# Optimization experiments

Hardware: AMD Instinct MI355X
Metric: run time of the kernel (lower is better)

Reference implementation:

```python
import jax, jax.numpy as jnp
import numpy as np

BETA = 0.5

def setup_inputs() -> dict:
    key = jax.random.key(0)
    ks = jax.random.split(key, 12)
    B, H, d, hid = 2048, 100, 128, 256
    item_num, region_num, dist_num = 100000, 1000, 16
    return {
        "history": jax.random.randint(ks[0], (B, H), 0, item_num),
        "target": jax.random.randint(ks[1], (B,), 0, item_num),
        "history_region": jax.random.randint(ks[2], (B, H), 0, region_num),
        "target_region": jax.random.randint(ks[3], (B,), 0, region_num),
        "target_distance": jax.random.uniform(ks[4], (B,), dtype=jnp.float32),
        "E_hist": jax.random.normal(ks[5], (item_num, d), dtype=jnp.float32) * 0.01,
        "E_tgt": jax.random.normal(ks[6], (item_num, d), dtype=jnp.float32) * 0.01,
        "E_reg": jax.random.normal(ks[7], (region_num, d), dtype=jnp.float32) * 0.01,
        "E_dist": jax.random.normal(ks[8], (dist_num, d), dtype=jnp.float32) * 0.01,
        "W1": jax.random.normal(ks[9], (hid, 2 * d), dtype=jnp.float32) * 0.05,
        "b1": jnp.zeros((hid,), dtype=jnp.float32),
        "w2": jax.random.normal(ks[10], (hid,), dtype=jnp.float32) * 0.05,
    }

def reference(history, target, history_region, target_region, target_distance,
              E_hist, E_tgt, E_reg, E_dist, W1, b1, w2):
    # history embeddings: [B,H,2d]
    hist = jnp.concatenate([E_hist[history], E_reg[history_region]], axis=-1)
    # target embeddings: [B,1,2d]
    tgt = jnp.concatenate([E_tgt[target], E_reg[target_region]], axis=-1)[:, None, :]
    x = hist * tgt                                   # [B,H,2d]
    a = jax.nn.relu(jnp.einsum('bhd,kd->bhk', x, W1) + b1)  # [B,H,hid]
    score = jnp.einsum('bhk,k->bh', a, w2)           # [B,H]
    # distance bias: scalar per batch element
    dist = jnp.sum(target_distance[:, None] * E_dist[0], axis=1)  # [B]
    exp_A = jnp.exp(score + dist[:, None])           # [B,H]
    mask = (history != target[:, None]).astype(exp_A.dtype)
    exp_A = exp_A * mask
    exp_sum = jnp.power(jnp.sum(exp_A, axis=-1), BETA)  # [B]
    attn = exp_A / exp_sum[:, None]                  # [B,H]
    # weighted inner product: sum_h sum_d attn*hist*tgt
    pred = jnp.sum(hist * attn[:, :, None] * tgt, axis=(1, 2))  # [B]
    return jax.nn.sigmoid(pred)
```

## Files before the change

### kernel.cpp

```cpp
#include <hip/hip_runtime.h>
#include <stdint.h>

typedef __attribute__((ext_vector_type(8))) short bf16x8;
typedef __attribute__((ext_vector_type(4))) float f32x4;

#define HH  100
#define DD  128
#define HID 256
#define NT  7

__device__ __forceinline__ unsigned short f2bf(float f) {
    unsigned int u = __float_as_uint(f);
    u += 0x7fffu + ((u >> 16) & 1u);
    return (unsigned short)(u >> 16);
}

__global__ void w1_pack(const float* __restrict__ W1, unsigned short* __restrict__ W1p) {
    int unit = blockIdx.x * 256 + threadIdx.x;
    int lane = unit & 63;
    int s    = (unit >> 6) & 7;
    int st   = unit >> 9;
    int col  = lane & 15, quad = lane >> 4;
    const float* src = W1 + (size_t)(st * 16 + col) * HID + s * 32 + quad * 8;
    union { unsigned short u[8]; bf16x8 v; } o;
    #pragma unroll
    for (int j = 0; j < 8; j++) o.u[j] = f2bf(src[j]);
    *(bf16x8*)(W1p + (size_t)unit * 8) = o.v;
}

__device__ __forceinline__ unsigned int cvt_pk_bf16(float lo, float hi) {
    unsigned int r;
    asm("v_cvt_pk_bf16_f32 %0, %1, %2" : "=v"(r) : "v"(lo), "v"(hi));
    return r;
}

#define CONSUME(V0, V1, S, AP, TGT, ACC) do {                                     \
    const float* tp_ = (TGT) + (S) * 32 + quad * 8;                               \
    float4 t0_ = *(const float4*)tp_, t1_ = *(const float4*)(tp_ + 4);            \
    float x0=(V0).x*t0_.x, x1=(V0).y*t0_.y, x2=(V0).z*t0_.z, x3=(V0).w*t0_.w;     \
    float x4=(V1).x*t1_.x, x5=(V1).y*t1_.y, x6=(V1).z*t1_.z, x7=(V1).w*t1_.w;     \
    (ACC) += (x0+x1)+(x2+x3)+((x4+x5)+(x6+x7));                                   \
    union { unsigned int u[4]; int4 v; } fb_;                                     \
    fb_.u[0]=cvt_pk_bf16(x0,x1); fb_.u[1]=cvt_pk_bf16(x2,x3);                     \
    fb_.u[2]=cvt_pk_bf16(x4,x5); fb_.u[3]=cvt_pk_bf16(x6,x7);                     \
    *(int4*)((AP) + (size_t)((S) * 64 + lane) * 8) = fb_.v;                       \
} while (0)

#define MFMA_PAIR(MM0, MM1) do {                                                  \
    int m0_ = (MM0); if (m0_ >= NT) m0_ -= NT;                                    \
    int m1_ = (MM1); if (m1_ >= NT) m1_ -= NT;                                    \
    const unsigned short* a0p_ = Ab + m0_ * 4096;                                 \
    const unsigned short* a1p_ = Ab + m1_ * 4096;                                 \
    f32x4 c00_={0,0,0,0}, c01_={0,0,0,0}, c10_={0,0,0,0}, c11_={0,0,0,0};         \
    _Pragma("unroll")                                                             \
    for (int s_ = 0; s_ < 8; s_++) {                                              \
        bf16x8 x0_ = *(const bf16x8*)(a0p_ + (size_t)(s_ * 64 + lane) * 8);       \
        bf16x8 x1_ = *(const bf16x8*)(a1p_ + (size_t)(s_ * 64 + lane) * 8);       \
        c00_ = __builtin_amdgcn_mfma_f32_16x16x32_bf16(w1f[s_],     x0_, c00_, 0,0,0); \
        c01_ = __builtin_amdgcn_mfma_f32_16x16x32_bf16(w1f[8 + s_], x0_, c01_, 0,0,0); \
        c10_ = __builtin_amdgcn_mfma_f32_16x16x32_bf16(w1f[s_],     x1_, c10_, 0,0,0); \
        c11_ = __builtin_amdgcn_mfma_f32_16x16x32_bf16(w1f[8 + s_], x1_, c11_, 0,0,0); \
    }                                                                             \
    float sp0_ = 0.f, sp1_ = 0.f;                                                 \
    _Pragma("unroll")                                                             \
    for (int r_ = 0; r_ < 4; r_++) {                                              \
        float z00_=c00_[r_]+bb0[r_], z01_=c01_[r_]+bb1[r_];                       \
        float z10_=c10_[r_]+bb0[r_], z11_=c11_[r_]+bb1[r_];                       \
        sp0_ += ((z00_>0.f)?z00_*ww0[r_]:0.f) + ((z01_>0.f)?z01_*ww1[r_]:0.f);    \
        sp1_ += ((z10_>0.f)?z10_*ww0[r_]:0.f) + ((z11_>0.f)?z11_*ww1[r_]:0.f);    \
    }                                                                             \
    sp0_ += __shfl_xor(sp0_, 16); sp0_ += __shfl_xor(sp0_, 32);                   \
    sp1_ += __shfl_xor(sp1_, 16); sp1_ += __shfl_xor(sp1_, 32);                   \
    if (quad == 0) {                                                              \
        scorep[wave][m0_ * 16 + col] = sp0_;                                      \
        scorep[wave][m1_ * 16 + col] = sp1_;                                      \
    }                                                                             \
} while (0)

#define MFMA_SINGLE(MM0) do {                                                     \
    int m0_ = (MM0); if (m0_ >= NT) m0_ -= NT;                                    \
    const unsigned short* a0p_ = Ab + m0_ * 4096;                                 \
    f32x4 c00_={0,0,0,0}, c01_={0,0,0,0};                                         \
    _Pragma("unroll")                                                             \
    for (int s_ = 0; s_ < 8; s_++) {                                              \
        bf16x8 x0_ = *(const bf16x8*)(a0p_ + (size_t)(s_ * 64 + lane) * 8);       \
        c00_ = __builtin_amdgcn_mfma_f32_16x16x32_bf16(w1f[s_],     x0_, c00_, 0,0,0); \
        c01_ = __builtin_amdgcn_mfma_f32_16x16x32_bf16(w1f[8 + s_], x0_, c01_, 0,0,0); \
    }                                                                             \
    float sp0_ = 0.f;                                                             \
    _Pragma("unroll")                                                             \
    for (int r_ = 0; r_ < 4; r_++) {                                              \
        float z00_=c00_[r_]+bb0[r_], z01_=c01_[r_]+bb1[r_];                       \
        sp0_ += ((z00_>0.f)?z00_*ww0[r_]:0.f) + ((z01_>0.f)?z01_*ww1[r_]:0.f);    \
    }                                                                             \
    sp0_ += __shfl_xor(sp0_, 16); sp0_ += __shfl_xor(sp0_, 32);                   \
    if (quad == 0) scorep[wave][m0_ * 16 + col] = sp0_;                           \
} while (0)

__global__ __launch_bounds__(512, 2) void nais_kernel(
    const int* __restrict__ history,
    const int* __restrict__ target,
    const int* __restrict__ history_region,
    const int* __restrict__ target_region,
    const float* __restrict__ target_distance,
    const float* __restrict__ E_hist,
    const float* __restrict__ E_tgt,
    const float* __restrict__ E_reg,
    const float* __restrict__ E_dist,
    const float* __restrict__ b1,
    const float* __restrict__ w2,
    const unsigned short* __restrict__ W1p,
    float* __restrict__ out,
    int Btot)
{
    __shared__ __align__(16) unsigned short As[2][NT * 4096];
    __shared__ __align__(16) float tgts3[3][HID];
    __shared__ __align__(16) float b1s[HID];
    __shared__ __align__(16) float w2s[HID];
    __shared__ __align__(16) int   hidx3[3][HH];
    __shared__ __align__(16) int   hreg3[3][HH];
    __shared__ __align__(16) float scorep[8][112];
    __shared__ __align__(16) float xsum2[2][112];
    __shared__ int   tgA[64];
    __shared__ int   trA[64];
    __shared__ float tdA[64];
    __shared__ float p12[2][4];
    __shared__ float s_sumE;

    const int t    = threadIdx.x;
    const int lane = t & 63;
    const int wave = t >> 6;
    const int col  = lane & 15;
    const int quad = lane >> 4;

    const int NB   = (Btot + gridDim.x - 1) / gridDim.x;
    const int base = blockIdx.x * NB;
    int cnt = Btot - base;
    if (cnt <= 0) return;
    if (cnt > NB) cnt = NB;

    if (t < cnt) {
        tgA[t] = target[base + t];
        trA[t] = target_region[base + t];
        tdA[t] = target_distance[base + t];
    }
    if (wave == 4) {
        *(float4*)(b1s + lane * 4) = *(const float4*)(b1 + lane * 4);
        *(float4*)(w2s + lane * 4) = *(const float4*)(w2 + lane * 4);
    }
    if (wave == 5) {
        float v = E_dist[lane] + E_dist[64 + lane];
        #pragma unroll
        for (int off = 32; off; off >>= 1) v += __shfl_xor(v, off);
        if (lane == 0) s_sumE = v;
    }
    __syncthreads();

    bf16x8 w1f[16];
    #pragma unroll
    for (int i = 0; i < 16; i++) {
        const int unit = ((2 * wave + (i >> 3)) * 8 + (i & 7)) * 64 + lane;
        w1f[i] = *(const bf16x8*)(W1p + (size_t)unit * 8);
    }
    #pragma unroll
    for (int i = 0; i < 16; i++) asm volatile("" : "+v"(w1f[i]));

    if (wave < 2 && wave < cnt) {
        const int em = base + wave;
        int4 mh = {0,0,0,0}, mr = {0,0,0,0};
        if (lane < 25)      mh = *(const int4*)(history + (size_t)em * HH + lane * 4);
        else if (lane < 50) mr = *(const int4*)(history_region + (size_t)em * HH + (lane - 25) * 4);
        const int tg2 = tgA[wave], tr2 = trA[wave];
        const float* tp2 = (lane < 32) ? (E_tgt + (size_t)tg2 * DD + lane * 4)
                                       : (E_reg + (size_t)tr2 * DD + (lane - 32) * 4);
        float4 mt4 = *(const float4*)tp2;
        if (lane < 25)      *(int4*)&hidx3[wave][lane * 4] = mh;
        else if (lane < 50) *(int4*)&hreg3[wave][(lane - 25) * 4] = mr;
        *(float4*)&tgts3[wave][lane * 4] = mt4;
    }
    __syncthreads();

    if (wave < NT) {
        const int row0 = wave * 16 + col;
        const int rc  = (row0 < HH) ? row0 : row0 - 64;
        const int ih  = hidx3[0][rc];
        const int ir  = hreg3[0][rc];
        const float* ph = E_hist + (size_t)ih * DD + quad * 8;
        const float* pr = E_reg  + (size_t)ir * DD + quad * 8;
        unsigned short* ap = &As[0][wave * 4096];
        float4 g[16];
        #pragma unroll
        for (int s = 0; s < 4; s++) {
            g[2*s]     = *(const float4*)(ph + s * 32);
            g[2*s + 1] = *(const float4*)(ph + s * 32 + 4);
            g[8 + 2*s] = *(const float4*)(pr + s * 32);
            g[9 + 2*s] = *(const float4*)(pr + s * 32 + 4);
        }
        float acc = 0.f;
        #pragma unroll
        for (int s = 0; s < 8; s++) CONSUME(g[2*s], g[2*s+1], s, ap, tgts3[0], acc);
        float v = acc;
        v += __shfl_xor(v, 16);
        v += __shfl_xor(v, 32);
        if (quad == 0) xsum2[0][row0] = v;
    }

    const int st0 = 2 * wave;
    const f32x4 bb0 = *(const f32x4*)&b1s[st0 * 16 + quad * 4];
    const f32x4 bb1 = *(const f32x4*)&b1s[st0 * 16 + 16 + quad * 4];
    const f32x4 ww0 = *(const f32x4*)&w2s[st0 * 16 + quad * 4];
    const f32x4 ww1 = *(const f32x4*)&w2s[st0 * 16 + 16 + quad * 4];

    __syncthreads();

    int cur = 0, cm = 0, nm = 1, n2 = 2;

    #pragma unroll 1
    for (int i = 0; i < cnt; i++) {
        const bool do_g = (i + 1 < cnt) && (wave < NT);
        const bool do_m = (i + 2 < cnt) && (wave == 7);

        float4 g[16];
        int row0 = 0;
        if (do_g) {
            row0 = wave * 16 + col;
            const int rc = (row0 < HH) ? row0 : row0 - 64;
            const int ih = hidx3[nm][rc];
            const int ir = hreg3[nm][rc];
            const float* ph = E_hist + (size_t)ih * DD + quad * 8;
            const float* pr = E_reg  + (size_t)ir * DD + quad * 8;
            #pragma unroll
            for (int s = 0; s < 4; s++) {
                g[2*s]     = *(const float4*)(ph + s * 32);
                g[2*s + 1] = *(const float4*)(ph + s * 32 + 4);
                g[8 + 2*s] = *(const float4*)(pr + s * 32);
                g[9 + 2*s] = *(const float4*)(pr + s * 32 + 4);
            }
        }
        int4 mh = {0,0,0,0}, mr4 = {0,0,0,0};
        float4 mt4 = {0.f, 0.f, 0.f, 0.f};
        if (do_m) {
            const int em = base + i + 2;
            if (lane < 25)      mh  = *(const int4*)(history + (size_t)em * HH + lane * 4);
            else if (lane < 50) mr4 = *(const int4*)(history_region + (size_t)em * HH + (lane - 25) * 4);
            const int tg2 = tgA[i + 2], tr2 = trA[i + 2];
            const float* tp2 = (lane < 32) ? (E_tgt + (size_t)tg2 * DD + lane * 4)
                                           : (E_reg + (size_t)tr2 * DD + (lane - 32) * 4);
            mt4 = *(const float4*)tp2;
        }

        const unsigned short* Ab = &As[cur][0];

        MFMA_PAIR(wave,     wave + 1);
        MFMA_PAIR(wave + 2, wave + 3);
        MFMA_PAIR(wave + 4, wave + 5);
        MFMA_SINGLE(wave + 6);

        __syncthreads();

        {
            float sc = 0.f;
            if (t < 112) {
                #pragma unroll
                for (int w = 0; w < 8; w++) sc += scorep[w][t];
            }
            float e1v = 0.f, e2v = 0.f;
            if (t < HH) {
                const float dist = tdA[i] * s_sumE;
                if (hidx3[cm][t] != tgA[i]) {
                    float e = expf(sc + dist);
                    e1v = e;
                    e2v = e * xsum2[cur][t];
                }
            }
            if (wave < 2) {
                #pragma unroll
                for (int off = 32; off; off >>= 1) {
                    e1v += __shfl_xor(e1v, off);
                    e2v += __shfl_xor(e2v, off);
                }
                if (lane == 0) {
                    p12[cur][wave]     = e1v;
                    p12[cur][2 + wave] = e2v;
                }
            }
            if (i > 0 && t == 128) {
                float s1 = p12[cur ^ 1][0] + p12[cur ^ 1][1];
                float s2 = p12[cur ^ 1][2] + p12[cur ^ 1][3];
                float pred = s2 / sqrtf(s1);
                out[base + i - 1] = 1.f / (1.f + expf(-pred));
            }
        }

        if (do_g) {
            unsigned short* An = &As[cur ^ 1][wave * 4096];
            const float* tgt = &tgts3[nm][0];
            float acc = 0.f;
            #pragma unroll
            for (int s = 0; s < 8; s++) CONSUME(g[2*s], g[2*s+1], s, An, tgt, acc);
            float v = acc;
            v += __shfl_xor(v, 16);
            v += __shfl_xor(v, 32);
            if (quad == 0) xsum2[cur ^ 1][row0] = v;
        } else if (do_m) {
            if (lane < 25)      *(int4*)&hidx3[n2][lane * 4] = mh;
            else if (lane < 50) *(int4*)&hreg3[n2][(lane - 25) * 4] = mr4;
            *(float4*)&tgts3[n2][lane * 4] = mt4;
        }

        __syncthreads();
        cur ^= 1;
        const int tmp = cm; cm = nm; nm = n2; n2 = tmp;
    }

    if (t == 0) {
        const int sl = (cnt - 1) & 1;
        float s1 = p12[sl][0] + p12[sl][1];
        float s2 = p12[sl][2] + p12[sl][3];
        float pred = s2 / sqrtf(s1);
        out[base + cnt - 1] = 1.f / (1.f + expf(-pred));
    }
}

extern "C" void kernel_launch(void* const* d_in, const int* in_sizes, int n_in,
                              void* d_out, int out_size, void* d_ws, size_t ws_size,
                              hipStream_t stream) {
    const int*   history         = (const int*)d_in[0];
    const int*   target          = (const int*)d_in[1];
    const int*   history_region  = (const int*)d_in[2];
    const int*   target_region   = (const int*)d_in[3];
    const float* target_distance = (const float*)d_in[4];
    const float* E_hist          = (const float*)d_in[5];
    const float* E_tgt           = (const float*)d_in[6];
    const float* E_reg           = (const float*)d_in[7];
    const float* E_dist          = (const float*)d_in[8];
    const float* W1              = (const float*)d_in[9];
    const float* b1              = (const float*)d_in[10];
    const float* w2              = (const float*)d_in[11];

    unsigned short* W1p = (unsigned short*)d_ws;
    const int B = in_sizes[1];

    int grid = (B + 7) / 8;
    if (grid > 256) grid = 256;

    w1_pack<<<32, 256, 0, stream>>>(W1, W1p);
    nais_kernel<<<grid, 512, 0, stream>>>(history, target, history_region, target_region,
                                          target_distance, E_hist, E_tgt, E_reg, E_dist,
                                          b1, w2, W1p, (float*)d_out, B);
}
```

Baseline: 185.8 us.

## Deepen software pipeline to one barrier per iteration and interleave MFMA with gather consume

```diff
diff --git a/kernel.cpp b/kernel.cpp
--- a/kernel.cpp
+++ b/kernel.cpp
@@ -72,8 +72,8 @@
     sp0_ += __shfl_xor(sp0_, 16); sp0_ += __shfl_xor(sp0_, 32);                   \
     sp1_ += __shfl_xor(sp1_, 16); sp1_ += __shfl_xor(sp1_, 32);                   \
     if (quad == 0) {                                                              \
-        scorep[wave][m0_ * 16 + col] = sp0_;                                      \
-        scorep[wave][m1_ * 16 + col] = sp1_;                                      \
+        scp[m0_ * 16 + col] = sp0_;                                               \
+        scp[m1_ * 16 + col] = sp1_;                                               \
     }                                                                             \
 } while (0)
 
@@ -94,7 +94,7 @@
         sp0_ += ((z00_>0.f)?z00_*ww0[r_]:0.f) + ((z01_>0.f)?z01_*ww1[r_]:0.f);    \
     }                                                                             \
     sp0_ += __shfl_xor(sp0_, 16); sp0_ += __shfl_xor(sp0_, 32);                   \
-    if (quad == 0) scorep[wave][m0_ * 16 + col] = sp0_;                           \
+    if (quad == 0) scp[m0_ * 16 + col] = sp0_;                                    \
 } while (0)
 
 __global__ __launch_bounds__(512, 2) void nais_kernel(
@@ -114,13 +114,13 @@
     int Btot)
 {
     __shared__ __align__(16) unsigned short As[2][NT * 4096];
-    __shared__ __align__(16) float tgts3[3][HID];
+    __shared__ __align__(16) float tgts4[4][HID];
     __shared__ __align__(16) float b1s[HID];
     __shared__ __align__(16) float w2s[HID];
-    __shared__ __align__(16) int   hidx3[3][HH];
-    __shared__ __align__(16) int   hreg3[3][HH];
-    __shared__ __align__(16) float scorep[8][112];
-    __shared__ __align__(16) float xsum2[2][112];
+    __shared__ __align__(16) int   hidx4[4][HH];
+    __shared__ __align__(16) int   hreg4[4][HH];
+    __shared__ __align__(16) float scorep[2][8][112];
+    __shared__ __align__(16) float xsumR[3][112];
     __shared__ int   tgA[64];
     __shared__ int   trA[64];
     __shared__ float tdA[64];
@@ -174,17 +174,17 @@
         const float* tp2 = (lane < 32) ? (E_tgt + (size_t)tg2 * DD + lane * 4)
                                        : (E_reg + (size_t)tr2 * DD + (lane - 32) * 4);
         float4 mt4 = *(const float4*)tp2;
-        if (lane < 25)      *(int4*)&hidx3[wave][lane * 4] = mh;
-        else if (lane < 50) *(int4*)&hreg3[wave][(lane - 25) * 4] = mr;
-        *(float4*)&tgts3[wave][lane * 4] = mt4;
+        if (lane < 25)      *(int4*)&hidx4[wave][lane * 4] = mh;
+        else if (lane < 50) *(int4*)&hreg4[wave][(lane - 25) * 4] = mr;
+        *(float4*)&tgts4[wave][lane * 4] = mt4;
     }
     __syncthreads();
 
     if (wave < NT) {
         const int row0 = wave * 16 + col;
         const int rc  = (row0 < HH) ? row0 : row0 - 64;
-        const int ih  = hidx3[0][rc];
-        const int ir  = hreg3[0][rc];
+        const int ih  = hidx4[0][rc];
+        const int ir  = hreg4[0][rc];
         const float* ph = E_hist + (size_t)ih * DD + quad * 8;
         const float* pr = E_reg  + (size_t)ir * DD + quad * 8;
         unsigned short* ap = &As[0][wave * 4096];
@@ -198,11 +198,11 @@
         }
         float acc = 0.f;
         #pragma unroll
-        for (int s = 0; s < 8; s++) CONSUME(g[2*s], g[2*s+1], s, ap, tgts3[0], acc);
+        for (int s = 0; s < 8; s++) CONSUME(g[2*s], g[2*s+1], s, ap, tgts4[0], acc);
         float v = acc;
         v += __shfl_xor(v, 16);
         v += __shfl_xor(v, 32);
-        if (quad == 0) xsum2[0][row0] = v;
+        if (quad == 0) xsumR[0][row0] = v;
     }
 
     const int st0 = 2 * wave;
@@ -213,20 +213,22 @@
 
     __syncthreads();
 
-    int cur = 0, cm = 0, nm = 1, n2 = 2;
-
     #pragma unroll 1
-    for (int i = 0; i < cnt; i++) {
+    for (int i = 0; i < cnt + 2; i++) {
+        const int  ii   = i & 1;
+        const bool do_f = (i < cnt);
         const bool do_g = (i + 1 < cnt) && (wave < NT);
         const bool do_m = (i + 2 < cnt) && (wave == 7);
+        const bool do_s = (i >= 1) && (i <= cnt);
 
         float4 g[16];
         int row0 = 0;
         if (do_g) {
+            const int ms = (i + 1) & 3;
             row0 = wave * 16 + col;
             const int rc = (row0 < HH) ? row0 : row0 - 64;
-            const int ih = hidx3[nm][rc];
-            const int ir = hreg3[nm][rc];
+            const int ih = hidx4[ms][rc];
+            const int ir = hreg4[ms][rc];
             const float* ph = E_hist + (size_t)ih * DD + quad * 8;
             const float* pr = E_reg  + (size_t)ir * DD + quad * 8;
             #pragma unroll
@@ -249,28 +251,52 @@
             mt4 = *(const float4*)tp2;
         }
 
-        const unsigned short* Ab = &As[cur][0];
-
-        MFMA_PAIR(wave,     wave + 1);
-        MFMA_PAIR(wave + 2, wave + 3);
-        MFMA_PAIR(wave + 4, wave + 5);
-        MFMA_SINGLE(wave + 6);
-
-        __syncthreads();
-
-        {
+        const unsigned short* Ab = &As[ii][0];
+        float*                scp = &scorep[ii][wave][0];
+        unsigned short*       An  = &As[ii ^ 1][wave * 4096];
+        const float*          tgt = &tgts4[(i + 1) & 3][0];
+        float acc = 0.f;
+
+        if (do_f) {
+            MFMA_PAIR(wave,     wave + 1);
+            MFMA_PAIR(wave + 2, wave + 3);
+        }
+        if (do_g) {
+            CONSUME(g[0], g[1], 0, An, tgt, acc);
+            CONSUME(g[2], g[3], 1, An, tgt, acc);
+            CONSUME(g[4], g[5], 2, An, tgt, acc);
+            CONSUME(g[6], g[7], 3, An, tgt, acc);
+        }
+        if (do_f) {
+            MFMA_PAIR(wave + 4, wave + 5);
+            MFMA_SINGLE(wave + 6);
+        }
+        if (do_g) {
+            CONSUME(g[8],  g[9],  4, An, tgt, acc);
+            CONSUME(g[10], g[11], 5, An, tgt, acc);
+            CONSUME(g[12], g[13], 6, An, tgt, acc);
+            CONSUME(g[14], g[15], 7, An, tgt, acc);
+            float v = acc;
+            v += __shfl_xor(v, 16);
+            v += __shfl_xor(v, 32);
+            if (quad == 0) xsumR[(i + 1) % 3][row0] = v;
+        }
+
+        if (do_s) {
+            const int ep = i - 1;
+            const float (*scR)[112] = scorep[ep & 1];
             float sc = 0.f;
             if (t < 112) {
                 #pragma unroll
-                for (int w = 0; w < 8; w++) sc += scorep[w][t];
+                for (int w = 0; w < 8; w++) sc += scR[w][t];
             }
             float e1v = 0.f, e2v = 0.f;
             if (t < HH) {
-                const float dist = tdA[i] * s_sumE;
-                if (hidx3[cm][t] != tgA[i]) {
-                    float e = expf(sc + dist);
-                    e1v = e;
-                    e2v = e * xsum2[cur][t];
+                const float dist = tdA[ep] * s_sumE;
+                if (hidx4[ep & 3][t] != tgA[ep]) {
+                    float ev = expf(sc + dist);
+                    e1v = ev;
+                    e2v = ev * xsumR[ep % 3][t];
                 }
             }
             if (wave < 2) {
@@ -280,45 +306,28 @@
                     e2v += __shfl_xor(e2v, off);
                 }
                 if (lane == 0) {
-                    p12[cur][wave]     = e1v;
-                    p12[cur][2 + wave] = e2v;
+                    p12[ep & 1][wave]     = e1v;
+                    p12[ep & 1][2 + wave] = e2v;
                 }
             }
-            if (i > 0 && t == 128) {
-                float s1 = p12[cur ^ 1][0] + p12[cur ^ 1][1];
-                float s2 = p12[cur ^ 1][2] + p12[cur ^ 1][3];
-                float pred = s2 / sqrtf(s1);
-                out[base + i - 1] = 1.f / (1.f + expf(-pred));
-            }
-        }
-
-        if (do_g) {
-            unsigned short* An = &As[cur ^ 1][wave * 4096];
-            const float* tgt = &tgts3[nm][0];
-            float acc = 0.f;
-            #pragma unroll
-            for (int s = 0; s < 8; s++) CONSUME(g[2*s], g[2*s+1], s, An, tgt, acc);
-            float v = acc;
-            v += __shfl_xor(v, 16);
-            v += __shfl_xor(v, 32);
-            if (quad == 0) xsum2[cur ^ 1][row0] = v;
-        } else if (do_m) {
-            if (lane < 25)      *(int4*)&hidx3[n2][lane * 4] = mh;
-            else if (lane < 50) *(int4*)&hreg3[n2][(lane - 25) * 4] = mr4;
-            *(float4*)&tgts3[n2][lane * 4] = mt4;
+        }
+
+        if (i >= 2 && t == 128) {
+            const int eo = i - 2;
+            float s1 = p12[eo & 1][0] + p12[eo & 1][1];
+            float s2 = p12[eo & 1][2] + p12[eo & 1][3];
+            float pred = s2 / sqrtf(s1);
+            out[base + eo] = 1.f / (1.f + expf(-pred));
+        }
+
+        if (do_m) {
+            const int ms = (i + 2) & 3;
+            if (lane < 25)      *(int4*)&hidx4[ms][lane * 4] = mh;
+            else if (lane < 50) *(int4*)&hreg4[ms][(lane - 25) * 4] = mr4;
+            *(float4*)&tgts4[ms][lane * 4] = mt4;
         }
 
         __syncthreads();
-        cur ^= 1;
-        const int tmp = cm; cm = nm; nm = n2; n2 = tmp;
-    }
-
-    if (t == 0) {
-        const int sl = (cnt - 1) & 1;
-        float s1 = p12[sl][0] + p12[sl][1];
-        float s2 = p12[sl][2] + p12[sl][3];
-        float pred = s2 / sqrtf(s1);
-        out[base + cnt - 1] = 1.f / (1.f + expf(-pred));
     }
 }
 
```

New measurement: 186.4 us. No clear change (+0.3%).

## Single-buffer A tile and split gather to raise occupancy to four blocks per CU

Applied to the files above, without the earlier changes.

```diff
diff --git a/kernel.cpp b/kernel.cpp
--- a/kernel.cpp
+++ b/kernel.cpp
@@ -97,7 +97,7 @@
     if (quad == 0) scorep[wave][m0_ * 16 + col] = sp0_;                           \
 } while (0)
 
-__global__ __launch_bounds__(512, 2) void nais_kernel(
+__global__ __launch_bounds__(512, 4) void nais_kernel(
     const int* __restrict__ history,
     const int* __restrict__ target,
     const int* __restrict__ history_region,
@@ -113,7 +113,7 @@
     float* __restrict__ out,
     int Btot)
 {
-    __shared__ __align__(16) unsigned short As[2][NT * 4096];
+    __shared__ __align__(16) unsigned short As[NT * 4096];
     __shared__ __align__(16) float tgts3[3][HID];
     __shared__ __align__(16) float b1s[HID];
     __shared__ __align__(16) float w2s[HID];
@@ -187,7 +187,7 @@
         const int ir  = hreg3[0][rc];
         const float* ph = E_hist + (size_t)ih * DD + quad * 8;
         const float* pr = E_reg  + (size_t)ir * DD + quad * 8;
-        unsigned short* ap = &As[0][wave * 4096];
+        unsigned short* ap = &As[wave * 4096];
         float4 g[16];
         #pragma unroll
         for (int s = 0; s < 4; s++) {
@@ -220,7 +220,8 @@
         const bool do_g = (i + 1 < cnt) && (wave < NT);
         const bool do_m = (i + 2 < cnt) && (wave == 7);
 
-        float4 g[16];
+        float4 gh[8];
+        const float* pr = nullptr;
         int row0 = 0;
         if (do_g) {
             row0 = wave * 16 + col;
@@ -228,13 +229,11 @@
             const int ih = hidx3[nm][rc];
             const int ir = hreg3[nm][rc];
             const float* ph = E_hist + (size_t)ih * DD + quad * 8;
-            const float* pr = E_reg  + (size_t)ir * DD + quad * 8;
+            pr = E_reg + (size_t)ir * DD + quad * 8;
             #pragma unroll
             for (int s = 0; s < 4; s++) {
-                g[2*s]     = *(const float4*)(ph + s * 32);
-                g[2*s + 1] = *(const float4*)(ph + s * 32 + 4);
-                g[8 + 2*s] = *(const float4*)(pr + s * 32);
-                g[9 + 2*s] = *(const float4*)(pr + s * 32 + 4);
+                gh[2*s]     = *(const float4*)(ph + s * 32);
+                gh[2*s + 1] = *(const float4*)(ph + s * 32 + 4);
             }
         }
         int4 mh = {0,0,0,0}, mr4 = {0,0,0,0};
@@ -249,7 +248,7 @@
             mt4 = *(const float4*)tp2;
         }
 
-        const unsigned short* Ab = &As[cur][0];
+        const unsigned short* Ab = &As[0];
 
         MFMA_PAIR(wave,     wave + 1);
         MFMA_PAIR(wave + 2, wave + 3);
@@ -257,6 +256,15 @@
         MFMA_SINGLE(wave + 6);
 
         __syncthreads();
+
+        float4 gr[8];
+        if (do_g) {
+            #pragma unroll
+            for (int s = 0; s < 4; s++) {
+                gr[2*s]     = *(const float4*)(pr + s * 32);
+                gr[2*s + 1] = *(const float4*)(pr + s * 32 + 4);
+            }
+        }
 
         {
             float sc = 0.f;
@@ -268,9 +276,9 @@
             if (t < HH) {
                 const float dist = tdA[i] * s_sumE;
                 if (hidx3[cm][t] != tgA[i]) {
-                    float e = expf(sc + dist);
-                    e1v = e;
-                    e2v = e * xsum2[cur][t];
+                    float ev = expf(sc + dist);
+                    e1v = ev;
+                    e2v = ev * xsum2[cur][t];
                 }
             }
             if (wave < 2) {
@@ -293,11 +301,17 @@
         }
 
         if (do_g) {
-            unsigned short* An = &As[cur ^ 1][wave * 4096];
+            unsigned short* An = &As[wave * 4096];
             const float* tgt = &tgts3[nm][0];
             float acc = 0.f;
-            #pragma unroll
-            for (int s = 0; s < 8; s++) CONSUME(g[2*s], g[2*s+1], s, An, tgt, acc);
+            CONSUME(gh[0], gh[1], 0, An, tgt, acc);
+            CONSUME(gh[2], gh[3], 1, An, tgt, acc);
+            CONSUME(gh[4], gh[5], 2, An, tgt, acc);
+            CONSUME(gh[6], gh[7], 3, An, tgt, acc);
+            CONSUME(gr[0], gr[1], 4, An, tgt, acc);
+            CONSUME(gr[2], gr[3], 5, An, tgt, acc);
+            CONSUME(gr[4], gr[5], 6, An, tgt, acc);
+            CONSUME(gr[6], gr[7], 7, An, tgt, acc);
             float v = acc;
             v += __shfl_xor(v, 16);
             v += __shfl_xor(v, 32);
@@ -341,8 +355,8 @@
     unsigned short* W1p = (unsigned short*)d_ws;
     const int B = in_sizes[1];
 
-    int grid = (B + 7) / 8;
-    if (grid > 256) grid = 256;
+    int grid = (B + 3) / 4;
+    if (grid > 512) grid = 512;
 
     w1_pack<<<32, 256, 0, stream>>>(W1, W1p);
     nais_kernel<<<grid, 512, 0, stream>>>(history, target, history_region, target_region,
```

Result: slower. 271.7 us (+46.3%).
